# Kernel tuning notes

Measured on AMD Instinct MI355X. Metric: run time of the kernel, lower is better.

Reference implementation:

```python
import jax, jax.numpy as jnp
import numpy as np

B, N, C, H = 2, 2048, 1024, 16
D = C // H  # head_dim = 64
ROPE_THETA = 500000.0
INIT_STD = 0.02


def setup_inputs() -> dict:
    key = jax.random.key(0)
    ks = jax.random.split(key, 6)
    hidden_states = jax.random.normal(ks[0], (B, N, C), dtype=jnp.float32)
    # rotary embeddings: standard llama-style, built from rope_theta
    inv_freq = jnp.asarray(1.0 / (ROPE_THETA ** (np.arange(0, D, 2, dtype=np.float32) / D)), jnp.float32)
    freqs = jnp.outer(jnp.arange(N, dtype=jnp.float32), inv_freq)  # (N, D/2)
    emb = jnp.concatenate([freqs, freqs], axis=-1)  # (N, D)
    cos = jnp.broadcast_to(jnp.cos(emb)[None], (B, N, D))
    sin = jnp.broadcast_to(jnp.sin(emb)[None], (B, N, D))
    Wq = jax.random.normal(ks[1], (C, C), jnp.float32) * INIT_STD
    Wk = jax.random.normal(ks[2], (C, C), jnp.float32) * INIT_STD
    Wv = jax.random.normal(ks[3], (C, C), jnp.float32) * INIT_STD
    Wo = jax.random.normal(ks[4], (C, C), jnp.float32) * INIT_STD
    return {"hidden_states": hidden_states, "cos": cos, "sin": sin,
            "Wq": Wq, "Wk": Wk, "Wv": Wv, "Wo": Wo}


def _rotate_half(x):
    x1, x2 = x[..., : D // 2], x[..., D // 2 :]
    return jnp.concatenate((-x2, x1), axis=-1)


def reference(hidden_states, cos, sin, Wq, Wk, Wv, Wo):
    scaling = D ** -0.5
    # projections; W stored as (in, out) so y = x @ W
    q = (hidden_states @ Wq) * scaling
    k = hidden_states @ Wk
    v = hidden_states @ Wv
    q = q.reshape(B, N, H, D)
    k = k.reshape(B, N, H, D)
    v = v.reshape(B, N, H, D)
    # RoPE, cos/sin broadcast over heads: (B,N,1,D)
    c = cos[:, :, None, :]
    s = sin[:, :, None, :]
    q = q * c + _rotate_half(q) * s
    k = k * c + _rotate_half(k) * s
    # causal SDPA (q already scaled)
    scores = jnp.einsum("bqhd,bkhd->bhqk", q, k)  # (B,H,N,N)
    causal = jnp.tril(jnp.ones((N, N), dtype=bool))
    scores = jnp.where(causal[None, None], scores, jnp.finfo(scores.dtype).min)
    probs = jax.nn.softmax(scores, axis=-1)
    out = jnp.einsum("bhqk,bkhd->bqhd", probs, v).reshape(B, N, C)
    return out @ Wo
```

## Files before the change

### kernel.cpp

```cpp
#include <hip/hip_runtime.h>
#include <hip/hip_bf16.h>

typedef __hip_bfloat16 bf16;
typedef __attribute__((ext_vector_type(8))) short short8;
typedef __attribute__((ext_vector_type(4))) short short4v;
typedef __attribute__((ext_vector_type(4))) float f32x4;

#define BB 2
#define NN 2048
#define CC 1024
#define HH 16
#define DD 64
#define MM (BB*NN)
#define QKVN 3072
#define LOG2E 1.44269504088896340736f

__device__ __forceinline__ void glds16(const void* g, void* l) {
    __builtin_amdgcn_global_load_lds((const __attribute__((address_space(1))) void*)g,
                                     (__attribute__((address_space(3))) void*)l, 16, 0, 0);
}
__device__ __forceinline__ short pkbf(float x) { bf16 t = (bf16)x; return *(short*)&t; }
__device__ __forceinline__ float b2f(short s) {
    return __uint_as_float(((unsigned)(unsigned short)s) << 16);
}

__global__ __launch_bounds__(256) void prep_fused(const float* __restrict__ hs,
                                                  const float* __restrict__ W0,
                                                  const float* __restrict__ W1,
                                                  const float* __restrict__ W2,
                                                  const float* __restrict__ W3,
                                                  bf16* __restrict__ hsb,
                                                  bf16* __restrict__ Wtqkv,
                                                  bf16* __restrict__ Wto) {
    __shared__ float t[32][33];
    const int bid = blockIdx.x;
    if (bid < 4096) {
        const int i = bid * 256 + threadIdx.x;
        float4 v = ((const float4*)hs)[i];
        short4v s;
        s.x = pkbf(v.x); s.y = pkbf(v.y); s.z = pkbf(v.z); s.w = pkbf(v.w);
        *((short4v*)hsb + i) = s;
    } else {
        const int b2 = bid - 4096;
        const int z = b2 >> 10;
        const float* W = z == 0 ? W0 : (z == 1 ? W1 : (z == 2 ? W2 : W3));
        bf16* dst = z < 3 ? Wtqkv + (size_t)z * CC * CC : Wto;
        const int bx = b2 & 31, by = (b2 >> 5) & 31;
        const int tx = threadIdx.x & 31, ty = threadIdx.x >> 5;
        const int x0 = bx * 32, y0 = by * 32;
        #pragma unroll
        for (int i = 0; i < 4; ++i)
            t[ty + i * 8][tx] = W[(size_t)(y0 + ty + i * 8) * CC + x0 + tx];
        __syncthreads();
        #pragma unroll
        for (int i = 0; i < 4; ++i)
            dst[(size_t)(x0 + ty + i * 8) * CC + y0 + tx] = (bf16)t[tx][ty + i * 8];
    }
}

template<int Nn, int MODE>
__global__ __launch_bounds__(256) void gemm4(const bf16* __restrict__ A,
                                             const bf16* __restrict__ Bt,
                                             void* __restrict__ Cout,
                                             const float* __restrict__ cosp,
                                             const float* __restrict__ sinp,
                                             bf16* __restrict__ VtOut) {
    __shared__ __align__(16) bf16 As[3][128 * 32];
    __shared__ __align__(16) bf16 Bs[3][128 * 32];
    const int tid = threadIdx.x, lane = tid & 63, wid = tid >> 6;
    const int wr = wid >> 1, wc = wid & 1, l16 = lane & 15, lg = lane >> 4;
    const int n0 = blockIdx.x * 128, m0 = blockIdx.y * 128;

    f32x4 acc[4][4];
    #pragma unroll
    for (int i = 0; i < 4; ++i)
        #pragma unroll
        for (int j = 0; j < 4; ++j) acc[i][j] = {0.f, 0.f, 0.f, 0.f};

    const int issue0 = wid * 2;
    const int sr0 = (issue0 * 1024 + lane * 16) >> 6;
    const int sc0 = ((issue0 * 1024 + lane * 16) & 63) >> 1;
    const int sr1 = ((issue0 + 1) * 1024 + lane * 16) >> 6;
    const int sc1 = (((issue0 + 1) * 1024 + lane * 16) & 63) >> 1;

    auto stage = [&](int k0, int bufi) {
        glds16(&A [(size_t)(m0 + sr0) * 1024 + k0 + sc0], (char*)&As[bufi][0] + issue0 * 1024);
        glds16(&Bt[(size_t)(n0 + sr0) * 1024 + k0 + sc0], (char*)&Bs[bufi][0] + issue0 * 1024);
        glds16(&A [(size_t)(m0 + sr1) * 1024 + k0 + sc1], (char*)&As[bufi][0] + (issue0 + 1) * 1024);
        glds16(&Bt[(size_t)(n0 + sr1) * 1024 + k0 + sc1], (char*)&Bs[bufi][0] + (issue0 + 1) * 1024);
    };

    stage(0, 0);
    stage(32, 1);
    int cur = 0, sb = 2;
    for (int t = 0; t < 32; ++t) {
        asm volatile("s_waitcnt vmcnt(4)" ::: "memory");
        __builtin_amdgcn_s_barrier();
        __builtin_amdgcn_sched_barrier(0);
        if (t + 2 < 32) stage((t + 2) * 32, sb);
        short8 af[4], bfr[4];
        #pragma unroll
        for (int i = 0; i < 4; ++i) af[i]  = *(const short8*)((char*)&As[cur][0] + (wr * 64 + i * 16 + l16) * 64 + lg * 16);
        #pragma unroll
        for (int j = 0; j < 4; ++j) bfr[j] = *(const short8*)((char*)&Bs[cur][0] + (wc * 64 + j * 16 + l16) * 64 + lg * 16);
        #pragma unroll
        for (int i = 0; i < 4; ++i)
            #pragma unroll
            for (int j = 0; j < 4; ++j)
                acc[i][j] = __builtin_amdgcn_mfma_f32_16x16x32_bf16(af[i], bfr[j], acc[i][j], 0, 0, 0);
        cur = (cur == 2) ? 0 : cur + 1;
        sb  = (sb  == 2) ? 0 : sb  + 1;
    }

    if (MODE == 1 && n0 >= 2 * CC) {
        #pragma unroll
        for (int i = 0; i < 4; ++i) {
            const int row0 = m0 + wr * 64 + i * 16 + lg * 4;
            const int bb = row0 >> 11, nn_ = row0 & (NN - 1);
            #pragma unroll
            for (int j = 0; j < 4; ++j) {
                const int col = n0 - 2 * CC + wc * 64 + j * 16 + l16;
                const int hh = col >> 6, d = col & 63;
                short4v s4;
                #pragma unroll
                for (int r = 0; r < 4; ++r) s4[r] = pkbf(acc[i][j][r]);
                *(short4v*)&VtOut[((size_t)(bb * HH + hh) * DD + d) * NN + nn_] = s4;
            }
        }
    } else if (MODE == 1) {
        const float qs = (n0 < CC) ? 0.125f * LOG2E : 1.0f;
        bf16* Cb = (bf16*)Cout;
        #pragma unroll
        for (int i = 0; i < 4; ++i)
            #pragma unroll
            for (int r = 0; r < 4; ++r) {
                const int row = m0 + wr * 64 + i * 16 + lg * 4 + r;
                #pragma unroll
                for (int j = 0; j < 2; ++j) {
                    const int d = j * 16 + l16;
                    const float cv = cosp[(size_t)row * DD + d];
                    const float sv = sinp[(size_t)row * DD + d];
                    const float x1 = acc[i][j][r];
                    const float x2 = acc[i][j + 2][r];
                    const size_t cbase = (size_t)row * QKVN + n0 + wc * 64 + j * 16 + l16;
                    Cb[cbase]      = (bf16)((x1 * cv - x2 * sv) * qs);
                    Cb[cbase + 32] = (bf16)((x2 * cv + x1 * sv) * qs);
                }
            }
    } else {
        float* Cf = (float*)Cout;
        #pragma unroll
        for (int i = 0; i < 4; ++i)
            #pragma unroll
            for (int r = 0; r < 4; ++r) {
                const int row = m0 + wr * 64 + i * 16 + lg * 4 + r;
                #pragma unroll
                for (int j = 0; j < 4; ++j)
                    Cf[(size_t)row * Nn + n0 + wc * 64 + j * 16 + l16] = acc[i][j][r];
            }
    }
}

__global__ __launch_bounds__(256) void flash_mfma6(const bf16* __restrict__ QKV,
                                                   const bf16* __restrict__ Vt,
                                                   bf16* __restrict__ PartA,
                                                   bf16* __restrict__ PartB,
                                                   bf16* __restrict__ PartC,
                                                   float2* __restrict__ Mlb) {
    __shared__ __align__(16) bf16 Ks[2][4096];
    __shared__ __align__(16) bf16 Vs[2][4096];
    const int tid = threadIdx.x, lane = tid & 63, wid = tid >> 6;
    const int l16 = lane & 15, lg = lane >> 4;
    const int bid = blockIdx.x;
    const int bh = bid & 31;
    const int slot = bid >> 5;
    const int qt = 31 - slot / 3;
    const int part = slot % 3;
    const int h = bh & (HH - 1), b = bh >> 4;
    const int wq0 = qt * 64 + wid * 16;
    const int nkt = qt + 1;
    const int t0 = (part * nkt) / 3;
    const int cnt = ((part + 1) * nkt) / 3 - t0;
    const int grow = b * NN + wq0 + l16;

    const bf16* Kbase = QKV + (size_t)b * NN * QKVN + CC + h * DD;
    const bf16* Vbase = Vt + (size_t)(b * HH + h) * DD * NN;

    short8 qf[2];
    #pragma unroll
    for (int ch = 0; ch < 2; ++ch)
        qf[ch] = *(const short8*)&QKV[(size_t)grow * QKVN + h * DD + ch * 32 + lg * 8];

    f32x4 o[4];
    #pragma unroll
    for (int dn = 0; dn < 4; ++dn) o[dn] = {0.f, 0.f, 0.f, 0.f};
    float mx = -1e30f, ls = 0.f;

    const int a0 = (wid * 2) * 1024 + lane * 16, a1 = a0 + 1024;
    const int r0 = a0 >> 7, c0 = ((a0 & 127) ^ ((r0 & 7) << 4)) >> 1;
    const int r1 = a1 >> 7, c1 = ((a1 & 127) ^ ((r1 & 7) << 4)) >> 1;
    const bf16* kp0 = Kbase + (size_t)(t0 * 64 + r0) * QKVN + c0;
    const bf16* kp1 = Kbase + (size_t)(t0 * 64 + r1) * QKVN + c1;
    const bf16* vp0 = Vbase + (size_t)r0 * NN + t0 * 64 + c0;
    const bf16* vp1 = Vbase + (size_t)r1 * NN + t0 * 64 + c1;
    char* ldsK = (char*)&Ks[0][0] + wid * 2048;
    char* ldsV = (char*)&Vs[0][0] + wid * 2048;

    auto stage = [&](int par) {
        glds16(kp0, ldsK + par * 8192);
        glds16(kp1, ldsK + par * 8192 + 1024);
        glds16(vp0, ldsV + par * 8192);
        glds16(vp1, ldsV + par * 8192 + 1024);
        kp0 += 64 * QKVN; kp1 += 64 * QKVN; vp0 += 64; vp1 += 64;
    };

    if (cnt > 0) stage(0);
    for (int i = 0; i < cnt; ++i) {
        __syncthreads();
        if (i + 1 < cnt) stage((i + 1) & 1);
        const int cur = i & 1;
        const int kt = t0 + i;
        const int k0 = kt * 64;

        f32x4 st[4];
        #pragma unroll
        for (int kc = 0; kc < 4; ++kc) st[kc] = {0.f, 0.f, 0.f, 0.f};
        __builtin_amdgcn_s_setprio(1);
        #pragma unroll
        for (int kc = 0; kc < 4; ++kc) {
            const int row = kc * 16 + l16;
            const char* rb = (const char*)&Ks[cur][0] + row * 128;
            const int sw = (row & 7) << 4;
            short8 kf0 = *(const short8*)(rb + ((lg * 16) ^ sw));
            short8 kf1 = *(const short8*)(rb + ((64 + lg * 16) ^ sw));
            st[kc] = __builtin_amdgcn_mfma_f32_16x16x32_bf16(kf0, qf[0], st[kc], 0, 0, 0);
            st[kc] = __builtin_amdgcn_mfma_f32_16x16x32_bf16(kf1, qf[1], st[kc], 0, 0, 0);
        }
        __builtin_amdgcn_s_setprio(0);

        if (kt == qt) {
            #pragma unroll
            for (int kc = 0; kc < 4; ++kc)
                #pragma unroll
                for (int r = 0; r < 4; ++r)
                    if (k0 + kc * 16 + lg * 4 + r > wq0 + l16) st[kc][r] = -1e30f;
        }

        float rm = fmaxf(fmaxf(st[0][0], st[0][1]), fmaxf(st[0][2], st[0][3]));
        #pragma unroll
        for (int kc = 1; kc < 4; ++kc)
            rm = fmaxf(rm, fmaxf(fmaxf(st[kc][0], st[kc][1]), fmaxf(st[kc][2], st[kc][3])));
        if (__any(rm > mx + 8.0f)) {
            float wmx = fmaxf(rm, __shfl_xor(rm, 16, 64));
            wmx = fmaxf(wmx, __shfl_xor(wmx, 32, 64));
            const float mn = fmaxf(mx, wmx);
            const float sc = __builtin_amdgcn_exp2f(mx - mn);
            ls *= sc;
            #pragma unroll
            for (int dn = 0; dn < 4; ++dn) {
                o[dn][0] *= sc; o[dn][1] *= sc; o[dn][2] *= sc; o[dn][3] *= sc;
            }
            mx = mn;
        }
        float rs = 0.f;
        #pragma unroll
        for (int kc = 0; kc < 4; ++kc)
            #pragma unroll
            for (int r = 0; r < 4; ++r) {
                const float p = __builtin_amdgcn_exp2f(st[kc][r] - mx);
                st[kc][r] = p; rs += p;
            }
        ls += rs;

        __builtin_amdgcn_s_setprio(1);
        #pragma unroll
        for (int kc = 0; kc < 4; ++kc) {
            short4v pf;
            pf[0] = pkbf(st[kc][0]); pf[1] = pkbf(st[kc][1]);
            pf[2] = pkbf(st[kc][2]); pf[3] = pkbf(st[kc][3]);
            #pragma unroll
            for (int dn = 0; dn < 4; ++dn) {
                const int row = dn * 16 + l16;
                short4v vf = *(const short4v*)((const char*)&Vs[cur][0] + row * 128
                                               + ((kc * 32 + lg * 8) ^ ((row & 7) << 4)));
                o[dn] = __builtin_amdgcn_mfma_f32_16x16x16bf16_1k(vf, pf, o[dn], 0, 0, 0);
            }
        }
        __builtin_amdgcn_s_setprio(0);
    }

    ls += __shfl_xor(ls, 16, 64);
    ls += __shfl_xor(ls, 32, 64);
    if (lg == 0) Mlb[((size_t)(part * MM) + grow) * HH + h] = make_float2(mx, ls);
    bf16* dst = part == 0 ? PartA : (part == 1 ? PartB : PartC);
    const size_t rowb = (size_t)grow * CC + h * DD;
    #pragma unroll
    for (int dn = 0; dn < 4; ++dn) {
        short4v s4;
        s4[0] = pkbf(o[dn][0]); s4[1] = pkbf(o[dn][1]);
        s4[2] = pkbf(o[dn][2]); s4[3] = pkbf(o[dn][3]);
        *(short4v*)&dst[rowb + dn * 16 + lg * 4] = s4;
    }
}

__global__ __launch_bounds__(256) void merge3(const bf16* __restrict__ pa,
                                              const bf16* __restrict__ pb,
                                              const bf16* __restrict__ pc,
                                              const float2* __restrict__ ml,
                                              bf16* __restrict__ outp) {
    const int idx = blockIdx.x * 256 + threadIdx.x;
    const int row = idx >> 7;
    const int h = (idx & 127) >> 3;
    const float2 a  = ml[(size_t)row * HH + h];
    const float2 b_ = ml[((size_t)MM + row) * HH + h];
    const float2 c  = ml[((size_t)2 * MM + row) * HH + h];
    const float M = fmaxf(fmaxf(a.x, b_.x), c.x);
    const float w0 = (a.y  > 0.f) ? __builtin_amdgcn_exp2f(a.x  - M) : 0.f;
    const float w1 = (b_.y > 0.f) ? __builtin_amdgcn_exp2f(b_.x - M) : 0.f;
    const float w2 = (c.y  > 0.f) ? __builtin_amdgcn_exp2f(c.x  - M) : 0.f;
    const float inv = 1.f / (a.y * w0 + b_.y * w1 + c.y * w2);
    const float f0 = w0 * inv, f1 = w1 * inv, f2 = w2 * inv;
    const size_t off = (size_t)idx * 8;
    short8 va = *(const short8*)(pa + off);
    short8 vb = *(const short8*)(pb + off);
    short8 vc = *(const short8*)(pc + off);
    short8 ov;
    #pragma unroll
    for (int e = 0; e < 8; ++e)
        ov[e] = pkbf(b2f(va[e]) * f0 + b2f(vb[e]) * f1 + b2f(vc[e]) * f2);
    *(short8*)(outp + off) = ov;
}

extern "C" void kernel_launch(void* const* d_in, const int* in_sizes, int n_in,
                              void* d_out, int out_size, void* d_ws, size_t ws_size,
                              hipStream_t stream) {
    const float* hs   = (const float*)d_in[0];
    const float* cosp = (const float*)d_in[1];
    const float* sinp = (const float*)d_in[2];
    const float* Wq   = (const float*)d_in[3];
    const float* Wk   = (const float*)d_in[4];
    const float* Wv   = (const float*)d_in[5];
    const float* Wo   = (const float*)d_in[6];
    float* out = (float*)d_out;

    char* ws = (char*)d_ws;
    bf16* hsb   = (bf16*)(ws);
    bf16* Wtqkv = (bf16*)(ws + (8  << 20));
    bf16* Wto   = (bf16*)(ws + (14 << 20));
    bf16* QKV   = (bf16*)(ws + (16 << 20));
    bf16* Vtb   = (bf16*)(ws + (40 << 20));
    bf16* Abuf  = hsb;
    float2* Mlb = (float2*)Wtqkv;
    bf16* PartB = (bf16*)out;
    bf16* PartC = (bf16*)out + (size_t)MM * CC;

    prep_fused<<<8192, 256, 0, stream>>>(hs, Wq, Wk, Wv, Wo, hsb, Wtqkv, Wto);

    gemm4<QKVN, 1><<<dim3(QKVN / 128, MM / 128), 256, 0, stream>>>(
        hsb, Wtqkv, QKV, cosp, sinp, Vtb);

    flash_mfma6<<<3072, 256, 0, stream>>>(QKV, Vtb, Abuf, PartB, PartC, Mlb);

    merge3<<<2048, 256, 0, stream>>>(Abuf, PartB, PartC, Mlb, Abuf);

    gemm4<CC, 2><<<dim3(CC / 128, MM / 128), 256, 0, stream>>>(
        Abuf, Wto, out, nullptr, nullptr, nullptr);
}
```

Measured before the change: 117.5 us.

## Enlarge flash attention query tile to 128 rows with two 16-row sub-tiles per wave

The flash attention kernel now processes 128 query rows per block (32 per wave, split into two 16-row MFMA sub-tiles) instead of 64. Each K/V tile staged in LDS is therefore reused for twice as many queries, which halves the K/V global-to-LDS traffic and the block count. Waves skip key tiles lying entirely above their causal diagonal. The cost is higher register pressure from doubled accumulators and score tiles, fewer blocks for load balancing, and idle waves on diagonal tiles.

Result: slower. 121.9 us (+3.8%).

```diff
diff --git a/kernel.cpp b/kernel.cpp
--- a/kernel.cpp
+++ b/kernel.cpp
@@ -161,7 +161,7 @@
     }
 }
 
-__global__ __launch_bounds__(256) void flash_mfma6(const bf16* __restrict__ QKV,
+__global__ __launch_bounds__(256) void flash_mfma9(const bf16* __restrict__ QKV,
                                                    const bf16* __restrict__ Vt,
                                                    bf16* __restrict__ PartA,
                                                    bf16* __restrict__ PartB,
@@ -174,27 +174,31 @@
     const int bid = blockIdx.x;
     const int bh = bid & 31;
     const int slot = bid >> 5;
-    const int qt = 31 - slot / 3;
+    const int qt = 15 - slot / 3;
     const int part = slot % 3;
     const int h = bh & (HH - 1), b = bh >> 4;
-    const int wq0 = qt * 64 + wid * 16;
-    const int nkt = qt + 1;
+    const int wq0 = qt * 128 + wid * 32;
+    const int nkt = 2 * qt + 2;
     const int t0 = (part * nkt) / 3;
     const int cnt = ((part + 1) * nkt) / 3 - t0;
-    const int grow = b * NN + wq0 + l16;
 
     const bf16* Kbase = QKV + (size_t)b * NN * QKVN + CC + h * DD;
     const bf16* Vbase = Vt + (size_t)(b * HH + h) * DD * NN;
 
-    short8 qf[2];
-    #pragma unroll
-    for (int ch = 0; ch < 2; ++ch)
-        qf[ch] = *(const short8*)&QKV[(size_t)grow * QKVN + h * DD + ch * 32 + lg * 8];
-
-    f32x4 o[4];
-    #pragma unroll
-    for (int dn = 0; dn < 4; ++dn) o[dn] = {0.f, 0.f, 0.f, 0.f};
-    float mx = -1e30f, ls = 0.f;
+    short8 qf[2][2];
+    #pragma unroll
+    for (int qm = 0; qm < 2; ++qm)
+        #pragma unroll
+        for (int ch = 0; ch < 2; ++ch)
+            qf[qm][ch] = *(const short8*)&QKV[(size_t)(b * NN + wq0 + qm * 16 + l16) * QKVN
+                                              + h * DD + ch * 32 + lg * 8];
+
+    f32x4 o[4][2];
+    #pragma unroll
+    for (int dn = 0; dn < 4; ++dn)
+        #pragma unroll
+        for (int qm = 0; qm < 2; ++qm) o[dn][qm] = {0.f, 0.f, 0.f, 0.f};
+    float mx[2] = {-1e30f, -1e30f}, ls[2] = {0.f, 0.f};
 
     const int a0 = (wid * 2) * 1024 + lane * 16, a1 = a0 + 1024;
     const int r0 = a0 >> 7, c0 = ((a0 & 127) ^ ((r0 & 7) << 4)) >> 1;
@@ -222,84 +226,108 @@
         const int kt = t0 + i;
         const int k0 = kt * 64;
 
-        f32x4 st[4];
-        #pragma unroll
-        for (int kc = 0; kc < 4; ++kc) st[kc] = {0.f, 0.f, 0.f, 0.f};
-        __builtin_amdgcn_s_setprio(1);
-        #pragma unroll
-        for (int kc = 0; kc < 4; ++kc) {
-            const int row = kc * 16 + l16;
-            const char* rb = (const char*)&Ks[cur][0] + row * 128;
-            const int sw = (row & 7) << 4;
-            short8 kf0 = *(const short8*)(rb + ((lg * 16) ^ sw));
-            short8 kf1 = *(const short8*)(rb + ((64 + lg * 16) ^ sw));
-            st[kc] = __builtin_amdgcn_mfma_f32_16x16x32_bf16(kf0, qf[0], st[kc], 0, 0, 0);
-            st[kc] = __builtin_amdgcn_mfma_f32_16x16x32_bf16(kf1, qf[1], st[kc], 0, 0, 0);
+        if (k0 <= wq0 + 31) {
+            f32x4 st[4][2];
+            #pragma unroll
+            for (int kc = 0; kc < 4; ++kc)
+                #pragma unroll
+                for (int qm = 0; qm < 2; ++qm) st[kc][qm] = {0.f, 0.f, 0.f, 0.f};
+            __builtin_amdgcn_s_setprio(1);
+            #pragma unroll
+            for (int kc = 0; kc < 4; ++kc) {
+                const int row = kc * 16 + l16;
+                const char* rb = (const char*)&Ks[cur][0] + row * 128;
+                const int sw = (row & 7) << 4;
+                short8 kf0 = *(const short8*)(rb + ((lg * 16) ^ sw));
+                short8 kf1 = *(const short8*)(rb + ((64 + lg * 16) ^ sw));
+                #pragma unroll
+                for (int qm = 0; qm < 2; ++qm) {
+                    st[kc][qm] = __builtin_amdgcn_mfma_f32_16x16x32_bf16(kf0, qf[qm][0], st[kc][qm], 0, 0, 0);
+                    st[kc][qm] = __builtin_amdgcn_mfma_f32_16x16x32_bf16(kf1, qf[qm][1], st[kc][qm], 0, 0, 0);
+                }
+            }
+            __builtin_amdgcn_s_setprio(0);
+
+            if (k0 + 63 > wq0) {
+                #pragma unroll
+                for (int kc = 0; kc < 4; ++kc)
+                    #pragma unroll
+                    for (int qm = 0; qm < 2; ++qm)
+                        #pragma unroll
+                        for (int r = 0; r < 4; ++r)
+                            if (k0 + kc * 16 + lg * 4 + r > wq0 + qm * 16 + l16)
+                                st[kc][qm][r] = -1e30f;
+            }
+
+            #pragma unroll
+            for (int qm = 0; qm < 2; ++qm) {
+                float rm = fmaxf(fmaxf(st[0][qm][0], st[0][qm][1]), fmaxf(st[0][qm][2], st[0][qm][3]));
+                #pragma unroll
+                for (int kc = 1; kc < 4; ++kc)
+                    rm = fmaxf(rm, fmaxf(fmaxf(st[kc][qm][0], st[kc][qm][1]),
+                                         fmaxf(st[kc][qm][2], st[kc][qm][3])));
+                if (__any(rm > mx[qm] + 8.0f)) {
+                    float wmx = fmaxf(rm, __shfl_xor(rm, 16, 64));
+                    wmx = fmaxf(wmx, __shfl_xor(wmx, 32, 64));
+                    const float mn = fmaxf(mx[qm], wmx);
+                    const float sc = __builtin_amdgcn_exp2f(mx[qm] - mn);
+                    ls[qm] *= sc;
+                    #pragma unroll
+                    for (int dn = 0; dn < 4; ++dn) {
+                        o[dn][qm][0] *= sc; o[dn][qm][1] *= sc;
+                        o[dn][qm][2] *= sc; o[dn][qm][3] *= sc;
+                    }
+                    mx[qm] = mn;
+                }
+                float rs = 0.f;
+                #pragma unroll
+                for (int kc = 0; kc < 4; ++kc)
+                    #pragma unroll
+                    for (int r = 0; r < 4; ++r) {
+                        const float p = __builtin_amdgcn_exp2f(st[kc][qm][r] - mx[qm]);
+                        st[kc][qm][r] = p; rs += p;
+                    }
+                ls[qm] += rs;
+            }
+
+            __builtin_amdgcn_s_setprio(1);
+            #pragma unroll
+            for (int kc = 0; kc < 4; ++kc) {
+                short4v pf[2];
+                #pragma unroll
+                for (int qm = 0; qm < 2; ++qm) {
+                    pf[qm][0] = pkbf(st[kc][qm][0]); pf[qm][1] = pkbf(st[kc][qm][1]);
+                    pf[qm][2] = pkbf(st[kc][qm][2]); pf[qm][3] = pkbf(st[kc][qm][3]);
+                }
+                #pragma unroll
+                for (int dn = 0; dn < 4; ++dn) {
+                    const int row = dn * 16 + l16;
+                    short4v vf = *(const short4v*)((const char*)&Vs[cur][0] + row * 128
+                                                   + ((kc * 32 + lg * 8) ^ ((row & 7) << 4)));
+                    o[dn][0] = __builtin_amdgcn_mfma_f32_16x16x16bf16_1k(vf, pf[0], o[dn][0], 0, 0, 0);
+                    o[dn][1] = __builtin_amdgcn_mfma_f32_16x16x16bf16_1k(vf, pf[1], o[dn][1], 0, 0, 0);
+                }
+            }
+            __builtin_amdgcn_s_setprio(0);
         }
-        __builtin_amdgcn_s_setprio(0);
-
-        if (kt == qt) {
-            #pragma unroll
-            for (int kc = 0; kc < 4; ++kc)
-                #pragma unroll
-                for (int r = 0; r < 4; ++r)
-                    if (k0 + kc * 16 + lg * 4 + r > wq0 + l16) st[kc][r] = -1e30f;
+    }
+
+    #pragma unroll
+    for (int qm = 0; qm < 2; ++qm) {
+        float l = ls[qm];
+        l += __shfl_xor(l, 16, 64);
+        l += __shfl_xor(l, 32, 64);
+        const int grow = b * NN + wq0 + qm * 16 + l16;
+        if (lg == 0) Mlb[((size_t)(part * MM) + grow) * HH + h] = make_float2(mx[qm], l);
+        bf16* dst = part == 0 ? PartA : (part == 1 ? PartB : PartC);
+        const size_t rowb = (size_t)grow * CC + h * DD;
+        #pragma unroll
+        for (int dn = 0; dn < 4; ++dn) {
+            short4v s4;
+            s4[0] = pkbf(o[dn][qm][0]); s4[1] = pkbf(o[dn][qm][1]);
+            s4[2] = pkbf(o[dn][qm][2]); s4[3] = pkbf(o[dn][qm][3]);
+            *(short4v*)&dst[rowb + dn * 16 + lg * 4] = s4;
         }
-
-        float rm = fmaxf(fmaxf(st[0][0], st[0][1]), fmaxf(st[0][2], st[0][3]));
-        #pragma unroll
-        for (int kc = 1; kc < 4; ++kc)
-            rm = fmaxf(rm, fmaxf(fmaxf(st[kc][0], st[kc][1]), fmaxf(st[kc][2], st[kc][3])));
-        if (__any(rm > mx + 8.0f)) {
-            float wmx = fmaxf(rm, __shfl_xor(rm, 16, 64));
-            wmx = fmaxf(wmx, __shfl_xor(wmx, 32, 64));
-            const float mn = fmaxf(mx, wmx);
-            const float sc = __builtin_amdgcn_exp2f(mx - mn);
-            ls *= sc;
-            #pragma unroll
-            for (int dn = 0; dn < 4; ++dn) {
-                o[dn][0] *= sc; o[dn][1] *= sc; o[dn][2] *= sc; o[dn][3] *= sc;
-            }
-            mx = mn;
-        }
-        float rs = 0.f;
-        #pragma unroll
-        for (int kc = 0; kc < 4; ++kc)
-            #pragma unroll
-            for (int r = 0; r < 4; ++r) {
-                const float p = __builtin_amdgcn_exp2f(st[kc][r] - mx);
-                st[kc][r] = p; rs += p;
-            }
-        ls += rs;
-
-        __builtin_amdgcn_s_setprio(1);
-        #pragma unroll
-        for (int kc = 0; kc < 4; ++kc) {
-            short4v pf;
-            pf[0] = pkbf(st[kc][0]); pf[1] = pkbf(st[kc][1]);
-            pf[2] = pkbf(st[kc][2]); pf[3] = pkbf(st[kc][3]);
-            #pragma unroll
-            for (int dn = 0; dn < 4; ++dn) {
-                const int row = dn * 16 + l16;
-                short4v vf = *(const short4v*)((const char*)&Vs[cur][0] + row * 128
-                                               + ((kc * 32 + lg * 8) ^ ((row & 7) << 4)));
-                o[dn] = __builtin_amdgcn_mfma_f32_16x16x16bf16_1k(vf, pf, o[dn], 0, 0, 0);
-            }
-        }
-        __builtin_amdgcn_s_setprio(0);
-    }
-
-    ls += __shfl_xor(ls, 16, 64);
-    ls += __shfl_xor(ls, 32, 64);
-    if (lg == 0) Mlb[((size_t)(part * MM) + grow) * HH + h] = make_float2(mx, ls);
-    bf16* dst = part == 0 ? PartA : (part == 1 ? PartB : PartC);
-    const size_t rowb = (size_t)grow * CC + h * DD;
-    #pragma unroll
-    for (int dn = 0; dn < 4; ++dn) {
-        short4v s4;
-        s4[0] = pkbf(o[dn][0]); s4[1] = pkbf(o[dn][1]);
-        s4[2] = pkbf(o[dn][2]); s4[3] = pkbf(o[dn][3]);
-        *(short4v*)&dst[rowb + dn * 16 + lg * 4] = s4;
     }
 }
 
@@ -359,7 +387,7 @@
     gemm4<QKVN, 1><<<dim3(QKVN / 128, MM / 128), 256, 0, stream>>>(
         hsb, Wtqkv, QKV, cosp, sinp, Vtb);
 
-    flash_mfma6<<<3072, 256, 0, stream>>>(QKV, Vtb, Abuf, PartB, PartC, Mlb);
+    flash_mfma9<<<1536, 256, 0, stream>>>(QKV, Vtb, Abuf, PartB, PartC, Mlb);
 
     merge3<<<2048, 256, 0, stream>>>(Abuf, PartB, PartC, Mlb, Abuf);
 
```
